# Optimization experiments

Measured on AMD Instinct MI355X. Metric: run time of the kernel, lower is better.

## Reference

```python
import jax, jax.numpy as jnp
import numpy as np

NH = 8       # num_heads
GROUPS = 32  # GroupNorm groups (guided-diffusion normalization())
EPS = 1e-5


def setup_inputs() -> dict:
    key = jax.random.key(0)
    ks = jax.random.split(key, 5)
    B, C, H, W = 16, 512, 32, 32
    return {
        "x": jax.random.normal(ks[0], (B, C, H, W), dtype=jnp.float32),
        "gn_scale": jnp.ones((C,), dtype=jnp.float32),
        "gn_bias": jnp.zeros((C,), dtype=jnp.float32),
        "w_qkv": jax.random.normal(ks[1], (3 * C, C), dtype=jnp.float32) * (C ** -0.5),
        "b_qkv": jax.random.normal(ks[2], (3 * C,), dtype=jnp.float32) * 0.02,
        "w_proj": jax.random.normal(ks[3], (C, C), dtype=jnp.float32) * (C ** -0.5),
        "b_proj": jax.random.normal(ks[4], (C,), dtype=jnp.float32) * 0.02,
    }


def reference(x, gn_scale, gn_bias, w_qkv, b_qkv, w_proj, b_proj):
    b, c, hh, ww = x.shape
    t = hh * ww
    ch = c // NH  # per-head channels
    xr = x.reshape(b, c, t)

    # GroupNorm(32, C) over (channels-in-group, spatial)
    xg = xr.reshape(b, GROUPS, c // GROUPS, t)
    mu = xg.mean(axis=(2, 3), keepdims=True)
    var = xg.var(axis=(2, 3), keepdims=True)
    h = ((xg - mu) * jax.lax.rsqrt(var + EPS)).reshape(b, c, t)
    h = h * gn_scale[None, :, None] + gn_bias[None, :, None]

    # conv1x1 qkv: [B, 3C, T]
    qkv = jnp.einsum('oc,bct->bot', w_qkv, h) + b_qkv[None, :, None]

    # legacy head split: reshape [B*NH, 3*ch, T] then split
    qkv = qkv.reshape(b * NH, 3 * ch, t)
    q, k, v = qkv[:, :ch], qkv[:, ch:2 * ch], qkv[:, 2 * ch:]

    scale = 1.0 / np.sqrt(np.sqrt(ch)).astype(np.float32)
    w = jnp.einsum('bct,bcs->bts', q * scale, k * scale)  # [B*NH, T, T]
    w = jax.nn.softmax(w.astype(jnp.float32), axis=-1).astype(qkv.dtype)
    a = jnp.einsum('bts,bcs->bct', w, v).reshape(b, c, t)

    # proj_out conv1x1 + residual
    out = jnp.einsum('oc,bct->bot', w_proj, a) + b_proj[None, :, None]
    return (xr + out).reshape(b, c, hh, ww)
```

## Files before the change

### kernel.cpp

```cpp
#include <hip/hip_runtime.h>
#include <stdint.h>

#define B_  16
#define C_  512
#define T_  1024
#define NH_ 8
#define O3_ 1536

typedef __bf16 bf16_t;
typedef bf16_t bf16x8 __attribute__((ext_vector_type(8)));
typedef float  f32x4  __attribute__((ext_vector_type(4)));
typedef float  f32x16 __attribute__((ext_vector_type(16)));
typedef unsigned short u16;
typedef unsigned int   u32;

#define QSCALE 0.18033688011112043f

__device__ inline u16 f2bf(float f) {
    union { float f; unsigned u; } v; v.f = f;
    unsigned r = v.u + 0x7FFF + ((v.u >> 16) & 1);
    return (u16)(r >> 16);
}
__device__ inline u32 pack2(float a, float b) {
    return (u32)f2bf(a) | ((u32)f2bf(b) << 16);
}

__global__ __launch_bounds__(256) void k_convert(const float* __restrict__ wq,
                                                 const float* __restrict__ wp,
                                                 u16* __restrict__ wq_b,
                                                 u16* __restrict__ wp_b) {
    int i = blockIdx.x * 256 + threadIdx.x;
    const int nq = O3_ * C_;
    if (i < nq) wq_b[i] = f2bf(wq[i]);
    else        wp_b[i - nq] = f2bf(wp[i - nq]);
}

__global__ __launch_bounds__(256) void k_gn(const float* __restrict__ x,
                                            const float* __restrict__ gsc,
                                            const float* __restrict__ gbi,
                                            u16* __restrict__ h_t) {
    __shared__ float red[8];
    int b = blockIdx.x >> 5, g = blockIdx.x & 31;
    int tid = threadIdx.x;
    const float4* src = (const float4*)(x + ((size_t)(b * C_ + g * 16)) * T_);
    float4 v[16];
    float s = 0.f, q = 0.f;
#pragma unroll
    for (int i = 0; i < 16; ++i) {
        v[i] = src[i * 256 + tid];
        s += v[i].x + v[i].y + v[i].z + v[i].w;
        q += v[i].x * v[i].x + v[i].y * v[i].y + v[i].z * v[i].z + v[i].w * v[i].w;
    }
#pragma unroll
    for (int m = 32; m; m >>= 1) { s += __shfl_xor(s, m); q += __shfl_xor(q, m); }
    int w = tid >> 6;
    if ((tid & 63) == 0) { red[w] = s; red[4 + w] = q; }
    __syncthreads();
    s = red[0] + red[1] + red[2] + red[3];
    q = red[4] + red[5] + red[6] + red[7];
    float mean = s * (1.f / 16384.f);
    float var  = q * (1.f / 16384.f) - mean * mean;
    float rstd = rsqrtf(var + 1e-5f);
    float sc[16], bi[16];
#pragma unroll
    for (int cc = 0; cc < 16; ++cc) {
        float gam = gsc[g * 16 + cc] * rstd;
        sc[cc] = gam;
        bi[cc] = gbi[g * 16 + cc] - mean * gam;
    }
#pragma unroll
    for (int j = 0; j < 4; ++j) {
        int t = tid * 4 + j;
        union { uint4 v4[2]; u16 u[16]; } ob;
#pragma unroll
        for (int cc = 0; cc < 16; ++cc) {
            float val = (&v[cc].x)[j];
            ob.u[cc] = f2bf(val * sc[cc] + bi[cc]);
        }
        uint4* dst = (uint4*)(h_t + ((size_t)(b * T_ + t)) * C_ + g * 16);
        dst[0] = ob.v4[0];
        dst[1] = ob.v4[1];
    }
}

__global__ __launch_bounds__(256) void k_qkv(const u16* __restrict__ h_t,
                                             const u16* __restrict__ wq_b,
                                             const float* __restrict__ bq,
                                             u16* __restrict__ q_t,
                                             u16* __restrict__ k_t,
                                             u16* __restrict__ v_t) {
    __shared__ __align__(16) u16 la[128 * 40];
    __shared__ __align__(16) u16 lb[128 * 40];
    int ob = blockIdx.x, tb = blockIdx.y, b = blockIdx.z;
    int tid = threadIdx.x, lane = tid & 63, w = tid >> 6;
    int wm = w >> 1, wn = w & 1;
    int t0 = tb * 128, o0 = ob * 128;
    const u16* srcA = h_t + ((size_t)b * T_ + t0) * C_;
    const u16* srcB = wq_b + (size_t)o0 * C_;
    int rowA = tid >> 2, kcol = (tid & 3) * 8;
    f32x4 acc[4][4] = {};
    for (int k0 = 0; k0 < C_; k0 += 32) {
        __syncthreads();
        *(uint4*)&la[rowA * 40 + kcol]        = *(const uint4*)&srcA[(size_t)rowA * C_ + k0 + kcol];
        *(uint4*)&la[(rowA + 64) * 40 + kcol] = *(const uint4*)&srcA[(size_t)(rowA + 64) * C_ + k0 + kcol];
        *(uint4*)&lb[rowA * 40 + kcol]        = *(const uint4*)&srcB[(size_t)rowA * C_ + k0 + kcol];
        *(uint4*)&lb[(rowA + 64) * 40 + kcol] = *(const uint4*)&srcB[(size_t)(rowA + 64) * C_ + k0 + kcol];
        __syncthreads();
        bf16x8 af[4], bfr[4];
        int rA = wm * 64 + (lane & 15);
        int rB = wn * 64 + (lane & 15);
        int kk = (lane >> 4) * 8;
#pragma unroll
        for (int m = 0; m < 4; ++m) af[m]  = *(const bf16x8*)&la[(rA + m * 16) * 40 + kk];
#pragma unroll
        for (int n = 0; n < 4; ++n) bfr[n] = *(const bf16x8*)&lb[(rB + n * 16) * 40 + kk];
#pragma unroll
        for (int m = 0; m < 4; ++m)
#pragma unroll
            for (int n = 0; n < 4; ++n)
                acc[m][n] = __builtin_amdgcn_mfma_f32_16x16x32_bf16(af[m], bfr[n], acc[m][n], 0, 0, 0);
    }
    int r0 = (lane >> 4) * 4;
#pragma unroll
    for (int n = 0; n < 4; ++n) {
        int o = o0 + wn * 64 + n * 16 + (lane & 15);
        float bqv = bq[o];
        int hh = o / 192;
        int rem = o - hh * 192;
#pragma unroll
        for (int m = 0; m < 4; ++m) {
#pragma unroll
            for (int r = 0; r < 4; ++r) {
                int t = t0 + wm * 64 + m * 16 + r0 + r;
                float fv = acc[m][n][r] + bqv;
                if (rem < 64)
                    q_t[((size_t)b * T_ + t) * C_ + hh * 64 + rem] = f2bf(fv * QSCALE);
                else if (rem < 128)
                    k_t[(((size_t)b * NH_ + hh) * T_ + t) * 64 + (rem - 64)] = f2bf(fv);
                else
                    v_t[(((size_t)b * NH_ + hh) * 64 + (rem - 128)) * T_ + t] = f2bf(fv);
            }
        }
    }
}

__global__ __launch_bounds__(512, 4) void k_attn(const u16* __restrict__ q_t,
                                                 const u16* __restrict__ k_t,
                                                 const u16* __restrict__ v_t,
                                                 u16* __restrict__ a_t) {
    __shared__ __align__(16) u16 kl[2][64 * 72];
    __shared__ __align__(16) u16 vl[2][64 * 72];
    __shared__ __align__(16) u16 pl[8][32 * 72];
    int bh = blockIdx.x, tb = blockIdx.y;
    int b = bh >> 3, h = bh & 7;
    int tid = threadIdx.x, lane = tid & 63, w = tid >> 6;
    int lo = lane & 31, hi = lane >> 5;
    int t0 = tb * 256;
    const u16* kbase = k_t + (size_t)bh * T_ * 64;
    const u16* vbase = v_t + (size_t)bh * 64 * T_;
    u16* pw = &pl[w][0];

    bf16x8 bq4[4];
    {
        int tq = t0 + w * 32 + lo;
        const u16* qrow = q_t + ((size_t)b * T_ + tq) * C_ + h * 64;
#pragma unroll
        for (int ks = 0; ks < 4; ++ks)
            bq4[ks] = *(const bf16x8*)&qrow[ks * 16 + hi * 8];
    }

    int srow = tid >> 3, schk = (tid & 7) * 8;
    int sofs = srow * 72 + schk;
    {
        uint4 kr = *(const uint4*)&kbase[(size_t)srow * 64 + schk];
        uint4 vr = *(const uint4*)&vbase[(size_t)srow * T_ + schk];
        *(uint4*)&kl[0][sofs] = kr;
        *(uint4*)&vl[0][sofs] = vr;
    }
    __syncthreads();

    f32x16 o0 = {}, o1 = {};
    float mrun = -1e30f, lrun = 0.f;

    int cur = 0;
    for (int it = 0; it < 16; ++it) {
        int s0g = it * 64;
        uint4 krg, vrg;
        if (it < 15) {
            krg = *(const uint4*)&kbase[(size_t)(s0g + 64 + srow) * 64 + schk];
            vrg = *(const uint4*)&vbase[(size_t)srow * T_ + s0g + 64 + schk];
        }
        f32x16 sa = {}, sb = {};
        __builtin_amdgcn_s_setprio(1);
#pragma unroll
        for (int ks = 0; ks < 4; ++ks) {
            bf16x8 ak0 = *(const bf16x8*)&kl[cur][(size_t)lo * 72 + ks * 16 + hi * 8];
            bf16x8 ak1 = *(const bf16x8*)&kl[cur][(size_t)(32 + lo) * 72 + ks * 16 + hi * 8];
            sa = __builtin_amdgcn_mfma_f32_32x32x16_bf16(ak0, bq4[ks], sa, 0, 0, 0);
            sb = __builtin_amdgcn_mfma_f32_32x32x16_bf16(ak1, bq4[ks], sb, 0, 0, 0);
        }
        __builtin_amdgcn_s_setprio(0);
        float mx = sa[0];
#pragma unroll
        for (int n = 1; n < 16; ++n) mx = fmaxf(mx, sa[n]);
#pragma unroll
        for (int n = 0; n < 16; ++n) mx = fmaxf(mx, sb[n]);
        mx = fmaxf(mx, __shfl_xor(mx, 32));
        if (!__all(mx <= mrun + 8.0f)) {
            float mnew = fmaxf(mrun, mx);
            float alpha = exp2f(mrun - mnew);
            mrun = mnew;
            lrun *= alpha;
            o0 *= alpha; o1 *= alpha;
        }
        float sum = 0.f;
#pragma unroll
        for (int n = 0; n < 16; ++n) { float p = exp2f(sa[n] - mrun); sa[n] = p; sum += p; }
#pragma unroll
        for (int n = 0; n < 16; ++n) { float p = exp2f(sb[n] - mrun); sb[n] = p; sum += p; }
        sum += __shfl_xor(sum, 32);
        lrun += sum;
#pragma unroll
        for (int g = 0; g < 4; ++g) {
            int sb0 = 8 * g + 4 * hi;
            *(u32*)&pw[lo * 72 + sb0]          = pack2(sa[4 * g],     sa[4 * g + 1]);
            *(u32*)&pw[lo * 72 + sb0 + 2]      = pack2(sa[4 * g + 2], sa[4 * g + 3]);
            *(u32*)&pw[lo * 72 + 32 + sb0]     = pack2(sb[4 * g],     sb[4 * g + 1]);
            *(u32*)&pw[lo * 72 + 32 + sb0 + 2] = pack2(sb[4 * g + 2], sb[4 * g + 3]);
        }
        bf16x8 pa[4];
#pragma unroll
        for (int ks = 0; ks < 4; ++ks)
            pa[ks] = *(const bf16x8*)&pw[lo * 72 + ks * 16 + hi * 8];
        __builtin_amdgcn_s_setprio(1);
#pragma unroll
        for (int ks = 0; ks < 4; ++ks) {
            bf16x8 av0 = *(const bf16x8*)&vl[cur][(size_t)lo * 72 + ks * 16 + hi * 8];
            bf16x8 av1 = *(const bf16x8*)&vl[cur][(size_t)(32 + lo) * 72 + ks * 16 + hi * 8];
            o0 = __builtin_amdgcn_mfma_f32_32x32x16_bf16(av0, pa[ks], o0, 0, 0, 0);
            o1 = __builtin_amdgcn_mfma_f32_32x32x16_bf16(av1, pa[ks], o1, 0, 0, 0);
        }
        __builtin_amdgcn_s_setprio(0);
        if (it < 15) {
            *(uint4*)&kl[cur ^ 1][sofs] = krg;
            *(uint4*)&vl[cur ^ 1][sofs] = vrg;
        }
        __syncthreads();
        cur ^= 1;
    }
    {
        float rl = 1.0f / lrun;
        int t = t0 + w * 32 + lo;
        u16* arow = a_t + ((size_t)b * T_ + t) * C_ + h * 64;
        const int cmap[8] = {0, 2, 8, 10, 16, 18, 24, 26};
#pragma unroll
        for (int m = 0; m < 8; ++m) {
            u32 w0 = pack2(o0[2 * m] * rl, o0[2 * m + 1] * rl);
            u32 w1 = pack2(o1[2 * m] * rl, o1[2 * m + 1] * rl);
            *(u32*)&arow[cmap[m] + 4 * hi]      = w0;
            *(u32*)&arow[32 + cmap[m] + 4 * hi] = w1;
        }
    }
}

__global__ __launch_bounds__(256) void k_proj(const u16* __restrict__ a_t,
                                              const u16* __restrict__ wp_b,
                                              const float* __restrict__ bp,
                                              const float* __restrict__ x,
                                              float* __restrict__ out) {
    __shared__ __align__(16) u16 la[128 * 40];
    __shared__ __align__(16) u16 lb[128 * 40];
    int tb = blockIdx.x, ob = blockIdx.y, b = blockIdx.z;
    int tid = threadIdx.x, lane = tid & 63, w = tid >> 6;
    int wm = w >> 1, wn = w & 1;
    int o0 = ob * 128, t0 = tb * 128;
    const u16* srcA = wp_b + (size_t)o0 * C_;
    const u16* srcB = a_t + ((size_t)b * T_ + t0) * C_;
    int rowA = tid >> 2, kcol = (tid & 3) * 8;
    f32x4 acc[4][4] = {};
    for (int k0 = 0; k0 < C_; k0 += 32) {
        __syncthreads();
        *(uint4*)&la[rowA * 40 + kcol]        = *(const uint4*)&srcA[(size_t)rowA * C_ + k0 + kcol];
        *(uint4*)&la[(rowA + 64) * 40 + kcol] = *(const uint4*)&srcA[(size_t)(rowA + 64) * C_ + k0 + kcol];
        *(uint4*)&lb[rowA * 40 + kcol]        = *(const uint4*)&srcB[(size_t)rowA * C_ + k0 + kcol];
        *(uint4*)&lb[(rowA + 64) * 40 + kcol] = *(const uint4*)&srcB[(size_t)(rowA + 64) * C_ + k0 + kcol];
        __syncthreads();
        bf16x8 af[4], bfr[4];
        int rA = wm * 64 + (lane & 15);
        int rB = wn * 64 + (lane & 15);
        int kk = (lane >> 4) * 8;
#pragma unroll
        for (int m = 0; m < 4; ++m) af[m]  = *(const bf16x8*)&la[(rA + m * 16) * 40 + kk];
#pragma unroll
        for (int n = 0; n < 4; ++n) bfr[n] = *(const bf16x8*)&lb[(rB + n * 16) * 40 + kk];
#pragma unroll
        for (int m = 0; m < 4; ++m)
#pragma unroll
            for (int n = 0; n < 4; ++n)
                acc[m][n] = __builtin_amdgcn_mfma_f32_16x16x32_bf16(af[m], bfr[n], acc[m][n], 0, 0, 0);
    }
    int r0 = (lane >> 4) * 4;
#pragma unroll
    for (int m = 0; m < 4; ++m) {
#pragma unroll
        for (int r = 0; r < 4; ++r) {
            int o = o0 + wm * 64 + m * 16 + r0 + r;
            float bpv = bp[o];
            const float* xrow = x + ((size_t)b * C_ + o) * T_;
            float* orow = out + ((size_t)b * C_ + o) * T_;
#pragma unroll
            for (int n = 0; n < 4; ++n) {
                int t = t0 + wn * 64 + n * 16 + (lane & 15);
                orow[t] = acc[m][n][r] + bpv + xrow[t];
            }
        }
    }
}

extern "C" void kernel_launch(void* const* d_in, const int* in_sizes, int n_in,
                              void* d_out, int out_size, void* d_ws, size_t ws_size,
                              hipStream_t stream) {
    (void)in_sizes; (void)n_in; (void)out_size; (void)ws_size;
    const float* x   = (const float*)d_in[0];
    const float* gsc = (const float*)d_in[1];
    const float* gbi = (const float*)d_in[2];
    const float* wq  = (const float*)d_in[3];
    const float* bq  = (const float*)d_in[4];
    const float* wp  = (const float*)d_in[5];
    const float* bp  = (const float*)d_in[6];
    float* out = (float*)d_out;
    char* ws = (char*)d_ws;

    u16* wq_b = (u16*)(ws);
    u16* wp_b = (u16*)(ws + 1572864);
    u16* h_t  = (u16*)(ws + 2097152);
    u16* q_t  = (u16*)(ws + 18874368);
    u16* k_t  = (u16*)(ws + 35651584);
    u16* v_t  = (u16*)(ws + 52428800);
    u16* a_t  = h_t;

    k_convert<<<dim3(4096), dim3(256), 0, stream>>>(wq, wp, wq_b, wp_b);
    k_gn<<<dim3(B_ * 32), dim3(256), 0, stream>>>(x, gsc, gbi, h_t);
    k_qkv<<<dim3(12, 8, B_), dim3(256), 0, stream>>>(h_t, wq_b, bq, q_t, k_t, v_t);
    k_attn<<<dim3(B_ * NH_, 4), dim3(512), 0, stream>>>(q_t, k_t, v_t, a_t);
    k_proj<<<dim3(8, 4, B_), dim3(256), 0, stream>>>(a_t, wp_b, bp, x, out);
}
```

Before: 174.2 us.

## Use direct global-to-LDS loads in GEMM kernels and specialize QKV epilogue

The QKV and projection GEMMs now stage tiles with global_load_lds (16-byte direct-to-LDS loads) instead of loading into registers and storing to shared memory. This drops the padded 40-element row stride for a dense 32-element layout. The QKV epilogue hoists the q/k/v branch to once per 16-column fragment, since a fragment never straddles a q/k/v boundary, which removes per-element division and branching. Float-to-bf16 conversion now uses the native __bf16 cast instead of manual rounding. The unpadded LDS layout may add bank conflicts on the fragment reads, and the direct-to-LDS loads still sit behind the same barriers with no double buffering.

```diff
diff --git a/kernel.cpp b/kernel.cpp
--- a/kernel.cpp
+++ b/kernel.cpp
@@ -17,12 +17,18 @@
 #define QSCALE 0.18033688011112043f
 
 __device__ inline u16 f2bf(float f) {
-    union { float f; unsigned u; } v; v.f = f;
-    unsigned r = v.u + 0x7FFF + ((v.u >> 16) & 1);
-    return (u16)(r >> 16);
+    union { __bf16 h; u16 u; } r; r.h = (__bf16)f; return r.u;
 }
 __device__ inline u32 pack2(float a, float b) {
-    return (u32)f2bf(a) | ((u32)f2bf(b) << 16);
+    union { u32 u; __bf16 h[2]; } r;
+    r.h[0] = (__bf16)a; r.h[1] = (__bf16)b;
+    return r.u;
+}
+
+__device__ inline void gl16(const u16* g, u16* l) {
+    __builtin_amdgcn_global_load_lds((const __attribute__((address_space(1))) void*)g,
+                                     (__attribute__((address_space(3))) void*)l,
+                                     16, 0, 0);
 }
 
 __global__ __launch_bounds__(256) void k_convert(const float* __restrict__ wq,
@@ -89,31 +95,31 @@
                                              u16* __restrict__ q_t,
                                              u16* __restrict__ k_t,
                                              u16* __restrict__ v_t) {
-    __shared__ __align__(16) u16 la[128 * 40];
-    __shared__ __align__(16) u16 lb[128 * 40];
+    __shared__ __align__(16) u16 la[128 * 32];
+    __shared__ __align__(16) u16 lb[128 * 32];
     int ob = blockIdx.x, tb = blockIdx.y, b = blockIdx.z;
     int tid = threadIdx.x, lane = tid & 63, w = tid >> 6;
     int wm = w >> 1, wn = w & 1;
     int t0 = tb * 128, o0 = ob * 128;
     const u16* srcA = h_t + ((size_t)b * T_ + t0) * C_;
     const u16* srcB = wq_b + (size_t)o0 * C_;
-    int rowA = tid >> 2, kcol = (tid & 3) * 8;
+    int grow = (lane >> 2), gcol = (lane & 3) * 8;
     f32x4 acc[4][4] = {};
     for (int k0 = 0; k0 < C_; k0 += 32) {
         __syncthreads();
-        *(uint4*)&la[rowA * 40 + kcol]        = *(const uint4*)&srcA[(size_t)rowA * C_ + k0 + kcol];
-        *(uint4*)&la[(rowA + 64) * 40 + kcol] = *(const uint4*)&srcA[(size_t)(rowA + 64) * C_ + k0 + kcol];
-        *(uint4*)&lb[rowA * 40 + kcol]        = *(const uint4*)&srcB[(size_t)rowA * C_ + k0 + kcol];
-        *(uint4*)&lb[(rowA + 64) * 40 + kcol] = *(const uint4*)&srcB[(size_t)(rowA + 64) * C_ + k0 + kcol];
+        gl16(&srcA[(size_t)(w * 16 + grow) * C_ + k0 + gcol],        &la[w * 512]);
+        gl16(&srcA[(size_t)(64 + w * 16 + grow) * C_ + k0 + gcol],   &la[(4 + w) * 512]);
+        gl16(&srcB[(size_t)(w * 16 + grow) * C_ + k0 + gcol],        &lb[w * 512]);
+        gl16(&srcB[(size_t)(64 + w * 16 + grow) * C_ + k0 + gcol],   &lb[(4 + w) * 512]);
         __syncthreads();
         bf16x8 af[4], bfr[4];
         int rA = wm * 64 + (lane & 15);
         int rB = wn * 64 + (lane & 15);
         int kk = (lane >> 4) * 8;
 #pragma unroll
-        for (int m = 0; m < 4; ++m) af[m]  = *(const bf16x8*)&la[(rA + m * 16) * 40 + kk];
-#pragma unroll
-        for (int n = 0; n < 4; ++n) bfr[n] = *(const bf16x8*)&lb[(rB + n * 16) * 40 + kk];
+        for (int m = 0; m < 4; ++m) af[m]  = *(const bf16x8*)&la[(rA + m * 16) * 32 + kk];
+#pragma unroll
+        for (int n = 0; n < 4; ++n) bfr[n] = *(const bf16x8*)&lb[(rB + n * 16) * 32 + kk];
 #pragma unroll
         for (int m = 0; m < 4; ++m)
 #pragma unroll
@@ -121,25 +127,40 @@
                 acc[m][n] = __builtin_amdgcn_mfma_f32_16x16x32_bf16(af[m], bfr[n], acc[m][n], 0, 0, 0);
     }
     int r0 = (lane >> 4) * 4;
+    int li = lane & 15;
 #pragma unroll
     for (int n = 0; n < 4; ++n) {
-        int o = o0 + wn * 64 + n * 16 + (lane & 15);
-        float bqv = bq[o];
-        int hh = o / 192;
-        int rem = o - hh * 192;
-#pragma unroll
-        for (int m = 0; m < 4; ++m) {
-#pragma unroll
-            for (int r = 0; r < 4; ++r) {
-                int t = t0 + wm * 64 + m * 16 + r0 + r;
-                float fv = acc[m][n][r] + bqv;
-                if (rem < 64)
-                    q_t[((size_t)b * T_ + t) * C_ + hh * 64 + rem] = f2bf(fv * QSCALE);
-                else if (rem < 128)
-                    k_t[(((size_t)b * NH_ + hh) * T_ + t) * 64 + (rem - 64)] = f2bf(fv);
-                else
-                    v_t[(((size_t)b * NH_ + hh) * 64 + (rem - 128)) * T_ + t] = f2bf(fv);
-            }
+        int obase = o0 + wn * 64 + n * 16;
+        int hh = obase / 192;
+        int rem0 = obase - hh * 192;
+        float bqv = bq[obase + li];
+        if (rem0 < 64) {
+            u16* dq = q_t + (size_t)b * T_ * C_ + hh * 64 + rem0 + li;
+#pragma unroll
+            for (int m = 0; m < 4; ++m)
+#pragma unroll
+                for (int r = 0; r < 4; ++r) {
+                    int t = t0 + wm * 64 + m * 16 + r0 + r;
+                    dq[(size_t)t * C_] = f2bf((acc[m][n][r] + bqv) * QSCALE);
+                }
+        } else if (rem0 < 128) {
+            u16* dk = k_t + ((size_t)b * NH_ + hh) * T_ * 64 + (rem0 - 64) + li;
+#pragma unroll
+            for (int m = 0; m < 4; ++m)
+#pragma unroll
+                for (int r = 0; r < 4; ++r) {
+                    int t = t0 + wm * 64 + m * 16 + r0 + r;
+                    dk[(size_t)t * 64] = f2bf(acc[m][n][r] + bqv);
+                }
+        } else {
+            u16* dv = v_t + (((size_t)b * NH_ + hh) * 64 + (rem0 - 128) + li) * T_;
+#pragma unroll
+            for (int m = 0; m < 4; ++m)
+#pragma unroll
+                for (int r = 0; r < 4; ++r) {
+                    int t = t0 + wm * 64 + m * 16 + r0 + r;
+                    dv[t] = f2bf(acc[m][n][r] + bqv);
+                }
         }
     }
 }
@@ -268,31 +289,31 @@
                                               const float* __restrict__ bp,
                                               const float* __restrict__ x,
                                               float* __restrict__ out) {
-    __shared__ __align__(16) u16 la[128 * 40];
-    __shared__ __align__(16) u16 lb[128 * 40];
+    __shared__ __align__(16) u16 la[128 * 32];
+    __shared__ __align__(16) u16 lb[128 * 32];
     int tb = blockIdx.x, ob = blockIdx.y, b = blockIdx.z;
     int tid = threadIdx.x, lane = tid & 63, w = tid >> 6;
     int wm = w >> 1, wn = w & 1;
     int o0 = ob * 128, t0 = tb * 128;
     const u16* srcA = wp_b + (size_t)o0 * C_;
     const u16* srcB = a_t + ((size_t)b * T_ + t0) * C_;
-    int rowA = tid >> 2, kcol = (tid & 3) * 8;
+    int grow = (lane >> 2), gcol = (lane & 3) * 8;
     f32x4 acc[4][4] = {};
     for (int k0 = 0; k0 < C_; k0 += 32) {
         __syncthreads();
-        *(uint4*)&la[rowA * 40 + kcol]        = *(const uint4*)&srcA[(size_t)rowA * C_ + k0 + kcol];
-        *(uint4*)&la[(rowA + 64) * 40 + kcol] = *(const uint4*)&srcA[(size_t)(rowA + 64) * C_ + k0 + kcol];
-        *(uint4*)&lb[rowA * 40 + kcol]        = *(const uint4*)&srcB[(size_t)rowA * C_ + k0 + kcol];
-        *(uint4*)&lb[(rowA + 64) * 40 + kcol] = *(const uint4*)&srcB[(size_t)(rowA + 64) * C_ + k0 + kcol];
+        gl16(&srcA[(size_t)(w * 16 + grow) * C_ + k0 + gcol],      &la[w * 512]);
+        gl16(&srcA[(size_t)(64 + w * 16 + grow) * C_ + k0 + gcol], &la[(4 + w) * 512]);
+        gl16(&srcB[(size_t)(w * 16 + grow) * C_ + k0 + gcol],      &lb[w * 512]);
+        gl16(&srcB[(size_t)(64 + w * 16 + grow) * C_ + k0 + gcol], &lb[(4 + w) * 512]);
         __syncthreads();
         bf16x8 af[4], bfr[4];
         int rA = wm * 64 + (lane & 15);
         int rB = wn * 64 + (lane & 15);
         int kk = (lane >> 4) * 8;
 #pragma unroll
-        for (int m = 0; m < 4; ++m) af[m]  = *(const bf16x8*)&la[(rA + m * 16) * 40 + kk];
-#pragma unroll
-        for (int n = 0; n < 4; ++n) bfr[n] = *(const bf16x8*)&lb[(rB + n * 16) * 40 + kk];
+        for (int m = 0; m < 4; ++m) af[m]  = *(const bf16x8*)&la[(rA + m * 16) * 32 + kk];
+#pragma unroll
+        for (int n = 0; n < 4; ++n) bfr[n] = *(const bf16x8*)&lb[(rB + n * 16) * 32 + kk];
 #pragma unroll
         for (int m = 0; m < 4; ++m)
 #pragma unroll
```

Result: faster. 151.4 us (-13.1%).
